# Performance work log

Measured on AMD Instinct MI355X. Metric: run time of the kernel, lower is better.

The kernel has to match this reference:

```python
import jax, jax.numpy as jnp
import numpy as np

HEADS = 12
LN_EPS = 1e-5


def setup_inputs() -> dict:
    B, S, D = 2, 2048, 768
    k = jax.random.key(0)
    ks = jax.random.split(k, 16)
    std = 0.02
    inp = {
        "key": jax.random.normal(ks[0], (B, S, D), jnp.float32),
        "query": jax.random.normal(ks[1], (B, S, D), jnp.float32),
        "value": jax.random.normal(ks[2], (B, S, D), jnp.float32),
        "mask": jax.random.randint(ks[3], (B, S, S), 0, 2).astype(bool),
        "Wk_w": jax.random.normal(ks[4], (D, D), jnp.float32) * std,
        "Wk_b": jnp.zeros((D,), jnp.float32),
        "Wq_w": jax.random.normal(ks[5], (D, D), jnp.float32) * std,
        "Wq_b": jnp.zeros((D,), jnp.float32),
        "Wv_w": jax.random.normal(ks[6], (D, D), jnp.float32) * std,
        "Wv_b": jnp.zeros((D,), jnp.float32),
        "Wc_w": jax.random.normal(ks[7], (D, D), jnp.float32) * std,
        "Wc_b": jnp.zeros((D,), jnp.float32),
        "ln_g": jnp.ones((D,), jnp.float32),
        "ln_b": jnp.zeros((D,), jnp.float32),
    }
    return inp


def _mha(key, query, value, mask, Wk_w, Wk_b, Wq_w, Wq_b, Wv_w, Wv_b,
         Wc_w, Wc_b, ln_g, ln_b):
    B, Sq, D = query.shape
    Sk = key.shape[1]
    H = HEADS
    hd = D // H
    scaler = np.float32(D ** 0.5)  # NOTE: source scales by sqrt(hidden_size), not sqrt(head_dim)

    # QKV projections (torch Linear: x @ W.T + b)
    hk = (key @ Wk_w.T + Wk_b).reshape(B, Sk, H, hd).transpose(2, 0, 1, 3)    # (H,B,Sk,hd)
    hq = (query @ Wq_w.T + Wq_b).reshape(B, Sq, H, hd).transpose(2, 0, 1, 3)  # (H,B,Sq,hd)
    hv = (value @ Wv_w.T + Wv_b).reshape(B, Sk, H, hd).transpose(2, 0, 1, 3)  # (H,B,Sk,hd)

    qk = jnp.einsum('hbqd,hbkd->hbqk', hq, hk) / scaler
    qk = jnp.where(mask[None], -jnp.inf, qk)  # mask repeated over heads in source
    attn = jax.nn.softmax(qk, axis=-1)        # dropout is identity in eval
    out = jnp.einsum('hbqk,hbkd->hbqd', attn, hv)  # (H,B,Sq,hd)

    # Faithful replication of source reshape chain:
    # (H*B,Sq,hd).view(B,H,Sq,hd).permute(1,2,0,3).view(B,Sq,D)
    out = out.reshape(B, H, Sq, hd)             # flat reinterpretation, head-major data
    out = jnp.transpose(out, (1, 2, 0, 3)).reshape(B, Sq, D)

    out = out @ Wc_w.T + Wc_b                   # Wconcat; dropout identity
    x = out + query                             # residual
    mu = jnp.mean(x, axis=-1, keepdims=True)
    var = jnp.mean((x - mu) ** 2, axis=-1, keepdims=True)
    return ln_g * (x - mu) / jnp.sqrt(var + LN_EPS) + ln_b


def reference(key, query, value, mask, Wk_w, Wk_b, Wq_w, Wq_b, Wv_w, Wv_b,
              Wc_w, Wc_b, ln_g, ln_b):
    return _mha(key, query, value, mask, Wk_w, Wk_b, Wq_w, Wq_b,
                Wv_w, Wv_b, Wc_w, Wc_b, ln_g, ln_b)
```

## Files before the change

kernel.cpp:

```cpp
#include <hip/hip_runtime.h>
#include <stdint.h>

typedef float v4f __attribute__((ext_vector_type(4)));
typedef short v8s __attribute__((ext_vector_type(8)));

#define AS1 __attribute__((address_space(1)))
#define AS3 __attribute__((address_space(3)))

__device__ __forceinline__ void load16_to_lds(const void* g, void* l) {
  __builtin_amdgcn_global_load_lds((AS1 void*)g, (AS3 void*)l, 16, 0, 0);
}

__device__ __forceinline__ float fexp2(float x) {
#if __has_builtin(__builtin_amdgcn_exp2f)
  return __builtin_amdgcn_exp2f(x);
#else
  return exp2f(x);
#endif
}

__device__ __forceinline__ unsigned short f2bf_rn(float f) {
  union { float f; uint32_t u; } v; v.f = f;
  return (unsigned short)((v.u + 0x8000u) >> 16);
}
__device__ __forceinline__ uint32_t pack_bf2(float x, float y) {
  union { float f; uint32_t u; } a, b; a.f = x; b.f = y;
  return __builtin_amdgcn_perm(b.u + 0x8000u, a.u + 0x8000u, 0x07060302u);
}

#define QSCALE 0.052058786f

__global__ __launch_bounds__(256) void conv_pack_kernel(
    const float* __restrict__ wk, const float* __restrict__ wq,
    const float* __restrict__ wv, const float* __restrict__ wc,
    const float* __restrict__ kin, const float* __restrict__ qin,
    const float* __restrict__ vin, const uint32_t* __restrict__ mask,
    unsigned short* __restrict__ dk, unsigned short* __restrict__ dq,
    unsigned short* __restrict__ dv, unsigned short* __restrict__ dc,
    unsigned short* __restrict__ dki, unsigned short* __restrict__ dqi,
    unsigned short* __restrict__ dvi, uint32_t* __restrict__ bits) {
  const int id = blockIdx.x;
  const int tid = threadIdx.x;
  if (id >= 11520) {
    const int xx = id - 11520;
    __shared__ int s_i32;
    if (tid == 0) s_i32 = 1;
    __syncthreads();
    if (mask[tid] > 1u) s_i32 = 0;
    __syncthreads();
    if (s_i32) {
      const int lane = tid & 63;
      const int gw = (xx * 256 + tid) >> 6;
#pragma unroll 4
      for (int it = 0; it < 32; ++it) {
        const size_t base = (size_t)gw * 2048 + it * 64;
        unsigned long long bal = __ballot(mask[base + lane] != 0u);
        if (lane == 0) *(unsigned long long*)&bits[base >> 5] = bal;
      }
    } else {
      const int wi = xx * 256 + tid;
      const uint32_t* p = mask + (size_t)wi * 8;
      uint32_t w = 0;
#pragma unroll
      for (int j8 = 0; j8 < 8; ++j8) {
        uint32_t u = p[j8];
#pragma unroll
        for (int k = 0; k < 4; ++k)
          w |= (((u >> (8 * k)) & 0xFFu) ? 1u : 0u) << (j8 * 4 + k);
      }
      bits[wi] = w;
    }
    return;
  }
  const float* s; unsigned short* d; float sc = 1.f; int x;
  if (id < 2304) {
    const int y = id / 576;
    x = id - y * 576;
    if (y == 0)      { s = wk; d = dk; }
    else if (y == 1) { s = wq; d = dq; sc = QSCALE; }
    else if (y == 2) { s = wv; d = dv; }
    else             { s = wc; d = dc; }
  } else {
    const int t = id - 2304;
    const int y = t / 3072;
    x = t - y * 3072;
    if (y == 0)      { s = kin; d = dki; }
    else if (y == 1) { s = qin; d = dqi; }
    else             { s = vin; d = dvi; }
  }
  const int i = x * 256 + tid;
  float4 f = ((const float4*)s)[i];
  uint2 o;
  o.x = pack_bf2(f.x * sc, f.y * sc);
  o.y = pack_bf2(f.z * sc, f.w * sc);
  ((uint2*)d)[i] = o;
}

__global__ __launch_bounds__(256, 3) void gemm_qkv_kernel(
    const unsigned short* __restrict__ qin, const unsigned short* __restrict__ kin,
    const unsigned short* __restrict__ vin,
    const unsigned short* __restrict__ wqb, const unsigned short* __restrict__ wkb,
    const unsigned short* __restrict__ wvb,
    const float* __restrict__ bq, const float* __restrict__ bk,
    const float* __restrict__ bv,
    unsigned short* __restrict__ Qb, unsigned short* __restrict__ Kb,
    unsigned short* __restrict__ Vt) {
  const int which = blockIdx.z;
  const unsigned short* A; const unsigned short* Wb; const float* bias;
  float bscale = 1.f;
  if (which == 0)      { A = qin; Wb = wqb; bias = bq; bscale = QSCALE; }
  else if (which == 1) { A = kin; Wb = wkb; bias = bk; }
  else                 { A = vin; Wb = wvb; bias = bv; }

  const int m0 = blockIdx.x * 128, n0 = blockIdx.y * 128;
  const int tid = threadIdx.x, lane = tid & 63, wid = tid >> 6;
  const int wm = wid >> 1, wn = wid & 1;
  const int l16 = lane & 15, quad = lane >> 4;

  __shared__ __align__(16) unsigned short As[2][128 * 32];
  __shared__ __align__(16) unsigned short Bs[2][128 * 32];

  v4f acc[4][4];
#pragma unroll
  for (int i = 0; i < 4; ++i)
#pragma unroll
    for (int j = 0; j < 4; ++j) { v4f z = {0.f, 0.f, 0.f, 0.f}; acc[i][j] = z; }

  const int c0 = wid * 128 + lane, c1 = wid * 128 + 64 + lane;
  const unsigned short* a0 = A + (size_t)(m0 + (c0 >> 2)) * 768 + (c0 & 3) * 8;
  const unsigned short* a1 = A + (size_t)(m0 + (c1 >> 2)) * 768 + (c1 & 3) * 8;
  const unsigned short* b0 = Wb + (size_t)(n0 + (c0 >> 2)) * 768 + (c0 & 3) * 8;
  const unsigned short* b1 = Wb + (size_t)(n0 + (c1 >> 2)) * 768 + (c1 & 3) * 8;

#define QKV_STAGE(k0, buf)                                         \
  do {                                                             \
    load16_to_lds(a0 + (k0), &As[buf][(wid * 128) * 8]);           \
    load16_to_lds(a1 + (k0), &As[buf][(wid * 128 + 64) * 8]);      \
    load16_to_lds(b0 + (k0), &Bs[buf][(wid * 128) * 8]);           \
    load16_to_lds(b1 + (k0), &Bs[buf][(wid * 128 + 64) * 8]);      \
  } while (0)

  QKV_STAGE(0, 0);
#pragma unroll 2
  for (int ks = 0; ks < 24; ++ks) {
    const int bufc = ks & 1;
    __syncthreads();
    v8s af[4], bf[4];
#pragma unroll
    for (int i = 0; i < 4; ++i)
      af[i] = *(const v8s*)&As[bufc][(wm * 64 + i * 16 + l16) * 32 + quad * 8];
#pragma unroll
    for (int j = 0; j < 4; ++j)
      bf[j] = *(const v8s*)&Bs[bufc][(wn * 64 + j * 16 + l16) * 32 + quad * 8];
    if (ks < 23) QKV_STAGE((ks + 1) * 32, bufc ^ 1);
#pragma unroll
    for (int i = 0; i < 4; ++i)
#pragma unroll
      for (int j = 0; j < 4; ++j)
        acc[i][j] = __builtin_amdgcn_mfma_f32_16x16x32_bf16(af[i], bf[j],
                                                            acc[i][j], 0, 0, 0);
  }
#undef QKV_STAGE

#pragma unroll
  for (int i = 0; i < 4; ++i) {
#pragma unroll
    for (int j = 0; j < 4; ++j) {
      const int mbase = m0 + wm * 64 + i * 16 + quad * 4;
      const int n = n0 + wn * 64 + j * 16 + l16;
      const float bv_ = bias[n] * bscale;
      if (which == 2) {
        const int bb = mbase >> 11, ss = mbase & 2047;
        uint2 pk;
        pk.x = pack_bf2(acc[i][j][0] + bv_, acc[i][j][1] + bv_);
        pk.y = pack_bf2(acc[i][j][2] + bv_, acc[i][j][3] + bv_);
        *(uint2*)&Vt[((size_t)bb * 768 + n) * 2048 + ss] = pk;
      } else {
        unsigned short* dst = (which == 0) ? Qb : Kb;
#pragma unroll
        for (int r = 0; r < 4; ++r)
          dst[(size_t)(mbase + r) * 768 + n] = f2bf_rn(acc[i][j][r] + bv_);
      }
    }
  }
}

__global__ __launch_bounds__(256, 4) void attn_kernel(
    const unsigned short* __restrict__ Qb, const unsigned short* __restrict__ Kb,
    const unsigned short* __restrict__ Vt, const uint32_t* __restrict__ mbits,
    unsigned short* __restrict__ X) {
  const int q0 = blockIdx.x * 64;
  const int h = blockIdx.y, b = blockIdx.z;
  const int tid = threadIdx.x, w = tid >> 6, lane = tid & 63;
  const int l16 = lane & 15, quad = lane >> 4, l7 = l16 & 7;

  __shared__ __align__(16) unsigned short Kl[2][64 * 64];
  __shared__ __align__(16) unsigned short Vl[2][64 * 64];
  __shared__ __align__(16) unsigned short Pl[4][16 * 64];

  v8s aq[2];
  {
    const unsigned short* qp =
        Qb + (size_t)(b * 2048 + q0 + w * 16 + l16) * 768 + h * 64 + quad * 8;
    aq[0] = *(const v8s*)qp;
    aq[1] = *(const v8s*)(qp + 32);
  }

  v4f o[4], ol;
#pragma unroll
  for (int nt = 0; nt < 4; ++nt) { v4f z = {0.f, 0.f, 0.f, 0.f}; o[nt] = z; }
  { v4f z = {0.f, 0.f, 0.f, 0.f}; ol = z; }

  v8s bones;
  {
    const short v1 = (l16 == 0) ? (short)0x3F80 : (short)0;
#pragma unroll
    for (int j = 0; j < 8; ++j) bones[j] = v1;
  }

  const int rsub = lane >> 3;
  const int csub = ((lane & 7) ^ rsub) * 8;
  const unsigned short* kg0 = Kb + (size_t)(b * 2048 + w * 16) * 768 + h * 64;
  const unsigned short* vg0 = Vt + (size_t)(b * 768 + h * 64 + w * 16) * 2048;
  const uint2* mp =
      (const uint2*)(mbits + (size_t)(b * 2048 + q0 + w * 16 + l16) * 64);

#define ATTN_STAGE(kk0, buf)                                                   \
  do {                                                                         \
    const unsigned short* kg = kg0 + (size_t)(kk0) * 768;                      \
    const unsigned short* vg = vg0 + (kk0);                                    \
    load16_to_lds(kg + (size_t)rsub * 768 + csub, &Kl[buf][(w * 16) * 64]);    \
    load16_to_lds(kg + (size_t)(8 + rsub) * 768 + csub,                        \
                  &Kl[buf][(w * 16 + 8) * 64]);                                \
    load16_to_lds(vg + (size_t)rsub * 2048 + csub, &Vl[buf][(w * 16) * 64]);   \
    load16_to_lds(vg + (size_t)(8 + rsub) * 2048 + csub,                       \
                  &Vl[buf][(w * 16 + 8) * 64]);                                \
  } while (0)

  ATTN_STAGE(0, 0);
  uint2 mreg = mp[0];
#pragma unroll 2
  for (int it = 0; it < 32; ++it) {
    const int bufc = it & 1;
    __syncthreads();

    v8s bk[2][4];
#pragma unroll
    for (int kt = 0; kt < 2; ++kt)
#pragma unroll
      for (int nt = 0; nt < 4; ++nt)
        bk[kt][nt] = *(const v8s*)&Kl[bufc][(nt * 16 + l16) * 64 +
                                           (((kt * 4 + quad) ^ l7) << 3)];
    uint2 mnext;
    if (it < 31) {
      ATTN_STAGE((it + 1) * 64, bufc ^ 1);
      mnext = mp[it + 1];
    }

    v4f sacc[4];
#pragma unroll
    for (int nt = 0; nt < 4; ++nt) { v4f z = {0.f, 0.f, 0.f, 0.f}; sacc[nt] = z; }
#pragma unroll
    for (int kt = 0; kt < 2; ++kt)
#pragma unroll
      for (int nt = 0; nt < 4; ++nt)
        sacc[nt] = __builtin_amdgcn_mfma_f32_16x16x32_bf16(bk[kt][nt], aq[kt],
                                                           sacc[nt], 0, 0, 0);

    const uint32_t u[4] = {mreg.x >> (quad * 4), mreg.x >> (quad * 4 + 16),
                           mreg.y >> (quad * 4), mreg.y >> (quad * 4 + 16)};
#pragma unroll
    for (int nt = 0; nt < 4; ++nt) {
      const float p0 = (u[nt] & 1u) ? 0.f : fexp2(sacc[nt][0]);
      const float p1 = ((u[nt] >> 1) & 1u) ? 0.f : fexp2(sacc[nt][1]);
      const float p2 = ((u[nt] >> 2) & 1u) ? 0.f : fexp2(sacc[nt][2]);
      const float p3 = ((u[nt] >> 3) & 1u) ? 0.f : fexp2(sacc[nt][3]);
      uint2 pk;
      pk.x = pack_bf2(p0, p1);
      pk.y = pack_bf2(p2, p3);
      const int elem =
          l16 * 64 + (((nt * 2 + (quad >> 1)) ^ l7) << 3) + (quad & 1) * 4;
      *(uint2*)&Pl[w][elem] = pk;
    }

#pragma unroll
    for (int kt = 0; kt < 2; ++kt) {
      const v8s ap = *(const v8s*)&Pl[w][l16 * 64 + (((kt * 4 + quad) ^ l7) << 3)];
#pragma unroll
      for (int nt = 0; nt < 4; ++nt) {
        const v8s bv = *(const v8s*)&Vl[bufc][(nt * 16 + l16) * 64 +
                                             (((kt * 4 + quad) ^ l7) << 3)];
        o[nt] = __builtin_amdgcn_mfma_f32_16x16x32_bf16(ap, bv, o[nt], 0, 0, 0);
      }
      ol = __builtin_amdgcn_mfma_f32_16x16x32_bf16(ap, bones, ol, 0, 0, 0);
    }
    mreg = mnext;
  }
#undef ATTN_STAGE

  const int hb2 = 2 * h + b;
  const int b2 = (hb2 >= 12) ? 1 : 0;
  const int h2 = hb2 - 12 * b2;
#pragma unroll
  for (int r = 0; r < 4; ++r) {
    const float lsum = __shfl(ol[r], quad * 16, 64);
    const float inv_l = 1.f / lsum;
    const int q = q0 + w * 16 + quad * 4 + r;
#pragma unroll
    for (int nt = 0; nt < 4; ++nt) {
      const int d = nt * 16 + l16;
      const size_t f = (size_t)h2 * 262144 + (size_t)q * 128 + b2 * 64 + d;
      X[f] = f2bf_rn(o[nt][r] * inv_l);
    }
  }
}

__global__ __launch_bounds__(256, 3) void gemm2_kernel(
    const unsigned short* __restrict__ X, const unsigned short* __restrict__ Wcb,
    const float* __restrict__ bc, const float* __restrict__ query,
    float* __restrict__ out) {
  const int m0 = blockIdx.x * 64, n0 = blockIdx.y * 128;
  const int tid = threadIdx.x, lane = tid & 63, wid = tid >> 6;
  const int wm = wid >> 1, wn = wid & 1;
  const int l16 = lane & 15, quad = lane >> 4;

  __shared__ __align__(16) unsigned short As[2][64 * 32];
  __shared__ __align__(16) unsigned short Bs[2][128 * 32];

  v4f acc[2][4];
#pragma unroll
  for (int i = 0; i < 2; ++i)
#pragma unroll
    for (int j = 0; j < 4; ++j) { v4f z = {0.f, 0.f, 0.f, 0.f}; acc[i][j] = z; }

  const int ca = tid;
  const unsigned short* a0 = X + (size_t)(m0 + (ca >> 2)) * 768 + (ca & 3) * 8;
  const int c0 = wid * 128 + lane, c1 = wid * 128 + 64 + lane;
  const unsigned short* b0 = Wcb + (size_t)(n0 + (c0 >> 2)) * 768 + (c0 & 3) * 8;
  const unsigned short* b1 = Wcb + (size_t)(n0 + (c1 >> 2)) * 768 + (c1 & 3) * 8;

#define G2_STAGE(k0, buf)                                        \
  do {                                                           \
    load16_to_lds(a0 + (k0), &As[buf][(wid * 64) * 8]);          \
    load16_to_lds(b0 + (k0), &Bs[buf][(wid * 128) * 8]);         \
    load16_to_lds(b1 + (k0), &Bs[buf][(wid * 128 + 64) * 8]);    \
  } while (0)

  G2_STAGE(0, 0);
#pragma unroll 2
  for (int ks = 0; ks < 24; ++ks) {
    const int bufc = ks & 1;
    __syncthreads();
    v8s af[2], bf[4];
#pragma unroll
    for (int i = 0; i < 2; ++i)
      af[i] = *(const v8s*)&As[bufc][(wm * 32 + i * 16 + l16) * 32 + quad * 8];
#pragma unroll
    for (int j = 0; j < 4; ++j)
      bf[j] = *(const v8s*)&Bs[bufc][(wn * 64 + j * 16 + l16) * 32 + quad * 8];
    if (ks < 23) G2_STAGE((ks + 1) * 32, bufc ^ 1);
#pragma unroll
    for (int i = 0; i < 2; ++i)
#pragma unroll
      for (int j = 0; j < 4; ++j)
        acc[i][j] = __builtin_amdgcn_mfma_f32_16x16x32_bf16(af[i], bf[j],
                                                            acc[i][j], 0, 0, 0);
  }
#undef G2_STAGE

#pragma unroll
  for (int i = 0; i < 2; ++i) {
#pragma unroll
    for (int j = 0; j < 4; ++j) {
      const int mbase = m0 + wm * 32 + i * 16 + quad * 4;
      const int n = n0 + wn * 64 + j * 16 + l16;
      const float bv_ = bc[n];
#pragma unroll
      for (int r = 0; r < 4; ++r) {
        const int m = mbase + r;
        out[(size_t)m * 768 + n] =
            acc[i][j][r] + bv_ + query[(size_t)m * 768 + n];
      }
    }
  }
}

__global__ __launch_bounds__(256) void ln_kernel(float* __restrict__ out,
                                                 const float* __restrict__ g,
                                                 const float* __restrict__ bta) {
  const int row = blockIdx.x;
  const int tid = threadIdx.x;
  float x[3];
  float s = 0.f, sq = 0.f;
#pragma unroll
  for (int k = 0; k < 3; ++k) {
    x[k] = out[(size_t)row * 768 + tid + k * 256];
    s += x[k];
    sq += x[k] * x[k];
  }
#pragma unroll
  for (int off = 1; off < 64; off <<= 1) {
    s += __shfl_xor(s, off, 64);
    sq += __shfl_xor(sq, off, 64);
  }
  __shared__ float ss[4], ssq[4];
  const int w = tid >> 6, lane = tid & 63;
  if (lane == 0) { ss[w] = s; ssq[w] = sq; }
  __syncthreads();
  s = ss[0] + ss[1] + ss[2] + ss[3];
  sq = ssq[0] + ssq[1] + ssq[2] + ssq[3];
  const float mu = s * (1.f / 768.f);
  const float var = sq * (1.f / 768.f) - mu * mu;
  const float rstd = rsqrtf(var + 1e-5f);
#pragma unroll
  for (int k = 0; k < 3; ++k) {
    const int cc = tid + k * 256;
    out[(size_t)row * 768 + cc] = g[cc] * (x[k] - mu) * rstd + bta[cc];
  }
}

extern "C" void kernel_launch(void* const* d_in, const int* in_sizes, int n_in,
                              void* d_out, int out_size, void* d_ws,
                              size_t ws_size, hipStream_t stream) {
  const float* key   = (const float*)d_in[0];
  const float* query = (const float*)d_in[1];
  const float* value = (const float*)d_in[2];
  const uint32_t* mask = (const uint32_t*)d_in[3];
  const float* Wk = (const float*)d_in[4];
  const float* bk = (const float*)d_in[5];
  const float* Wq = (const float*)d_in[6];
  const float* bq = (const float*)d_in[7];
  const float* Wv = (const float*)d_in[8];
  const float* bv = (const float*)d_in[9];
  const float* Wc = (const float*)d_in[10];
  const float* bc = (const float*)d_in[11];
  const float* lng = (const float*)d_in[12];
  const float* lnb = (const float*)d_in[13];

  char* ws = (char*)d_ws;
  uint32_t*       mbits = (uint32_t*)(ws);
  unsigned short* Wkb = (unsigned short*)(ws + 0x100000);
  unsigned short* Wqb = (unsigned short*)(ws + 0x220000);
  unsigned short* Wvb = (unsigned short*)(ws + 0x340000);
  unsigned short* Wcb = (unsigned short*)(ws + 0x460000);
  unsigned short* Qb  = (unsigned short*)(ws + 0x600000);
  unsigned short* Kb  = (unsigned short*)(ws + 0xC00000);
  unsigned short* Vt  = (unsigned short*)(ws + 0x1200000);
  unsigned short* X   = (unsigned short*)(ws + 0x1800000);
  unsigned short* Kin = (unsigned short*)d_out;
  unsigned short* Qin = (unsigned short*)d_out + 3145728;
  unsigned short* Vin = X;
  float* out = (float*)d_out;

  conv_pack_kernel<<<dim3(12544), dim3(256), 0, stream>>>(
      Wk, Wq, Wv, Wc, key, query, value, mask,
      Wkb, Wqb, Wvb, Wcb, Kin, Qin, Vin, mbits);
  gemm_qkv_kernel<<<dim3(32, 6, 3), dim3(256), 0, stream>>>(
      Qin, Kin, Vin, Wqb, Wkb, Wvb, bq, bk, bv, Qb, Kb, Vt);
  attn_kernel<<<dim3(32, 12, 2), dim3(256), 0, stream>>>(Qb, Kb, Vt, mbits, X);
  gemm2_kernel<<<dim3(64, 6), dim3(256), 0, stream>>>(X, Wcb, bc, query, out);
  ln_kernel<<<dim3(4096), dim3(256), 0, stream>>>(out, lng, lnb);
}
```

Baseline: 241.2 us.

## Fuse fp32-to-bf16 conversion and mask packing into QKV and output GEMMs

Removes the separate conversion kernel. The QKV and output-projection GEMMs now read fp32 activations and weights straight from global memory into registers, convert them to bf16 and store them into LDS, with a register-prefetched double buffer. Mask bit-packing moves into an extra z-slice of the QKV grid. For V the operand roles are swapped so the transposed Vt is written along contiguous rows. This saves one launch and a full bf16 round trip through memory. In exchange the GEMM mainloops do more register and VALU work, lose the async global-to-LDS loads, and Vt is now written as scalar 16-bit stores.

```diff
diff --git a/kernel.cpp b/kernel.cpp
--- a/kernel.cpp
+++ b/kernel.cpp
@@ -30,90 +30,57 @@
 
 #define QSCALE 0.052058786f
 
-__global__ __launch_bounds__(256) void conv_pack_kernel(
-    const float* __restrict__ wk, const float* __restrict__ wq,
-    const float* __restrict__ wv, const float* __restrict__ wc,
-    const float* __restrict__ kin, const float* __restrict__ qin,
-    const float* __restrict__ vin, const uint32_t* __restrict__ mask,
-    unsigned short* __restrict__ dk, unsigned short* __restrict__ dq,
-    unsigned short* __restrict__ dv, unsigned short* __restrict__ dc,
-    unsigned short* __restrict__ dki, unsigned short* __restrict__ dqi,
-    unsigned short* __restrict__ dvi, uint32_t* __restrict__ bits) {
-  const int id = blockIdx.x;
+__global__ __launch_bounds__(256, 3) void gemm_qkv_kernel(
+    const float* __restrict__ qin, const float* __restrict__ kin,
+    const float* __restrict__ vin,
+    const float* __restrict__ Wq, const float* __restrict__ Wk,
+    const float* __restrict__ Wv,
+    const float* __restrict__ bq, const float* __restrict__ bk,
+    const float* __restrict__ bv, const uint32_t* __restrict__ mask,
+    unsigned short* __restrict__ Qb, unsigned short* __restrict__ Kb,
+    unsigned short* __restrict__ Vt, uint32_t* __restrict__ bits) {
   const int tid = threadIdx.x;
-  if (id >= 11520) {
-    const int xx = id - 11520;
+  if (blockIdx.z == 3) {
     __shared__ int s_i32;
     if (tid == 0) s_i32 = 1;
     __syncthreads();
     if (mask[tid] > 1u) s_i32 = 0;
     __syncthreads();
-    if (s_i32) {
-      const int lane = tid & 63;
-      const int gw = (xx * 256 + tid) >> 6;
+    const int lane = tid & 63;
+    for (int g = blockIdx.x + 32 * blockIdx.y; g < 1024; g += 192) {
+      if (s_i32) {
+        const int gw = (g * 256 + tid) >> 6;
 #pragma unroll 4
-      for (int it = 0; it < 32; ++it) {
-        const size_t base = (size_t)gw * 2048 + it * 64;
-        unsigned long long bal = __ballot(mask[base + lane] != 0u);
-        if (lane == 0) *(unsigned long long*)&bits[base >> 5] = bal;
+        for (int it2 = 0; it2 < 32; ++it2) {
+          const size_t base = (size_t)gw * 2048 + it2 * 64;
+          unsigned long long bal = __ballot(mask[base + lane] != 0u);
+          if (lane == 0) *(unsigned long long*)&bits[base >> 5] = bal;
+        }
+      } else {
+        const int wi = g * 256 + tid;
+        const uint32_t* p = mask + (size_t)wi * 8;
+        uint32_t w = 0;
+#pragma unroll
+        for (int j8 = 0; j8 < 8; ++j8) {
+          uint32_t u = p[j8];
+#pragma unroll
+          for (int k = 0; k < 4; ++k)
+            w |= (((u >> (8 * k)) & 0xFFu) ? 1u : 0u) << (j8 * 4 + k);
+        }
+        bits[wi] = w;
       }
-    } else {
-      const int wi = xx * 256 + tid;
-      const uint32_t* p = mask + (size_t)wi * 8;
-      uint32_t w = 0;
-#pragma unroll
-      for (int j8 = 0; j8 < 8; ++j8) {
-        uint32_t u = p[j8];
-#pragma unroll
-        for (int k = 0; k < 4; ++k)
-          w |= (((u >> (8 * k)) & 0xFFu) ? 1u : 0u) << (j8 * 4 + k);
-      }
-      bits[wi] = w;
     }
     return;
   }
-  const float* s; unsigned short* d; float sc = 1.f; int x;
-  if (id < 2304) {
-    const int y = id / 576;
-    x = id - y * 576;
-    if (y == 0)      { s = wk; d = dk; }
-    else if (y == 1) { s = wq; d = dq; sc = QSCALE; }
-    else if (y == 2) { s = wv; d = dv; }
-    else             { s = wc; d = dc; }
-  } else {
-    const int t = id - 2304;
-    const int y = t / 3072;
-    x = t - y * 3072;
-    if (y == 0)      { s = kin; d = dki; }
-    else if (y == 1) { s = qin; d = dqi; }
-    else             { s = vin; d = dvi; }
-  }
-  const int i = x * 256 + tid;
-  float4 f = ((const float4*)s)[i];
-  uint2 o;
-  o.x = pack_bf2(f.x * sc, f.y * sc);
-  o.y = pack_bf2(f.z * sc, f.w * sc);
-  ((uint2*)d)[i] = o;
-}
-
-__global__ __launch_bounds__(256, 3) void gemm_qkv_kernel(
-    const unsigned short* __restrict__ qin, const unsigned short* __restrict__ kin,
-    const unsigned short* __restrict__ vin,
-    const unsigned short* __restrict__ wqb, const unsigned short* __restrict__ wkb,
-    const unsigned short* __restrict__ wvb,
-    const float* __restrict__ bq, const float* __restrict__ bk,
-    const float* __restrict__ bv,
-    unsigned short* __restrict__ Qb, unsigned short* __restrict__ Kb,
-    unsigned short* __restrict__ Vt) {
+
   const int which = blockIdx.z;
-  const unsigned short* A; const unsigned short* Wb; const float* bias;
-  float bscale = 1.f;
-  if (which == 0)      { A = qin; Wb = wqb; bias = bq; bscale = QSCALE; }
-  else if (which == 1) { A = kin; Wb = wkb; bias = bk; }
-  else                 { A = vin; Wb = wvb; bias = bv; }
+  const float* A; const float* W; const float* bias; float wsc = 1.f;
+  if (which == 0)      { A = qin; W = Wq; bias = bq; wsc = QSCALE; }
+  else if (which == 1) { A = kin; W = Wk; bias = bk; }
+  else                 { A = vin; W = Wv; bias = bv; }
 
   const int m0 = blockIdx.x * 128, n0 = blockIdx.y * 128;
-  const int tid = threadIdx.x, lane = tid & 63, wid = tid >> 6;
+  const int lane = tid & 63, wid = tid >> 6;
   const int wm = wid >> 1, wn = wid & 1;
   const int l16 = lane & 15, quad = lane >> 4;
 
@@ -126,57 +93,98 @@
 #pragma unroll
     for (int j = 0; j < 4; ++j) { v4f z = {0.f, 0.f, 0.f, 0.f}; acc[i][j] = z; }
 
-  const int c0 = wid * 128 + lane, c1 = wid * 128 + 64 + lane;
-  const unsigned short* a0 = A + (size_t)(m0 + (c0 >> 2)) * 768 + (c0 & 3) * 8;
-  const unsigned short* a1 = A + (size_t)(m0 + (c1 >> 2)) * 768 + (c1 & 3) * 8;
-  const unsigned short* b0 = Wb + (size_t)(n0 + (c0 >> 2)) * 768 + (c0 & 3) * 8;
-  const unsigned short* b1 = Wb + (size_t)(n0 + (c1 >> 2)) * 768 + (c1 & 3) * 8;
-
-#define QKV_STAGE(k0, buf)                                         \
-  do {                                                             \
-    load16_to_lds(a0 + (k0), &As[buf][(wid * 128) * 8]);           \
-    load16_to_lds(a1 + (k0), &As[buf][(wid * 128 + 64) * 8]);      \
-    load16_to_lds(b0 + (k0), &Bs[buf][(wid * 128) * 8]);           \
-    load16_to_lds(b1 + (k0), &Bs[buf][(wid * 128 + 64) * 8]);      \
+  const float* pA[2]; const float* pW[2]; int offs[2];
+#pragma unroll
+  for (int i = 0; i < 2; ++i) {
+    const int c = tid + i * 256;
+    const int row = c >> 2, col8 = (c & 3) * 8;
+    pA[i] = A + (size_t)(m0 + row) * 768 + col8;
+    pW[i] = W + (size_t)(n0 + row) * 768 + col8;
+    offs[i] = row * 32 + col8;
+  }
+
+  float4 fa[2][2], fw[2][2];
+#define QKV_LOAD(k0)                                      \
+  do {                                                    \
+    _Pragma("unroll") for (int i = 0; i < 2; ++i) {       \
+      fa[i][0] = *(const float4*)(pA[i] + (k0));          \
+      fa[i][1] = *(const float4*)(pA[i] + (k0) + 4);      \
+      fw[i][0] = *(const float4*)(pW[i] + (k0));          \
+      fw[i][1] = *(const float4*)(pW[i] + (k0) + 4);      \
+    }                                                     \
   } while (0)
-
-  QKV_STAGE(0, 0);
+#define QKV_STORE(buf)                                                   \
+  do {                                                                   \
+    _Pragma("unroll") for (int i = 0; i < 2; ++i) {                      \
+      uint4 oa, ow;                                                      \
+      oa.x = pack_bf2(fa[i][0].x, fa[i][0].y);                           \
+      oa.y = pack_bf2(fa[i][0].z, fa[i][0].w);                           \
+      oa.z = pack_bf2(fa[i][1].x, fa[i][1].y);                           \
+      oa.w = pack_bf2(fa[i][1].z, fa[i][1].w);                           \
+      ow.x = pack_bf2(fw[i][0].x * wsc, fw[i][0].y * wsc);               \
+      ow.y = pack_bf2(fw[i][0].z * wsc, fw[i][0].w * wsc);               \
+      ow.z = pack_bf2(fw[i][1].x * wsc, fw[i][1].y * wsc);               \
+      ow.w = pack_bf2(fw[i][1].z * wsc, fw[i][1].w * wsc);               \
+      *(uint4*)&As[buf][offs[i]] = oa;                                   \
+      *(uint4*)&Bs[buf][offs[i]] = ow;                                   \
+    }                                                                    \
+  } while (0)
+
+  QKV_LOAD(0);
+  QKV_STORE(0);
+  QKV_LOAD(32);
 #pragma unroll 2
   for (int ks = 0; ks < 24; ++ks) {
     const int bufc = ks & 1;
     __syncthreads();
     v8s af[4], bf[4];
+    const unsigned short* Abase = (which == 2) ? Bs[bufc] : As[bufc];
+    const unsigned short* Bbase = (which == 2) ? As[bufc] : Bs[bufc];
 #pragma unroll
     for (int i = 0; i < 4; ++i)
-      af[i] = *(const v8s*)&As[bufc][(wm * 64 + i * 16 + l16) * 32 + quad * 8];
+      af[i] = *(const v8s*)&Abase[(wm * 64 + i * 16 + l16) * 32 + quad * 8];
 #pragma unroll
     for (int j = 0; j < 4; ++j)
-      bf[j] = *(const v8s*)&Bs[bufc][(wn * 64 + j * 16 + l16) * 32 + quad * 8];
-    if (ks < 23) QKV_STAGE((ks + 1) * 32, bufc ^ 1);
+      bf[j] = *(const v8s*)&Bbase[(wn * 64 + j * 16 + l16) * 32 + quad * 8];
+    if (ks < 23) QKV_STORE(bufc ^ 1);
 #pragma unroll
     for (int i = 0; i < 4; ++i)
 #pragma unroll
       for (int j = 0; j < 4; ++j)
         acc[i][j] = __builtin_amdgcn_mfma_f32_16x16x32_bf16(af[i], bf[j],
                                                             acc[i][j], 0, 0, 0);
-  }
-#undef QKV_STAGE
-
-#pragma unroll
-  for (int i = 0; i < 4; ++i) {
-#pragma unroll
-    for (int j = 0; j < 4; ++j) {
-      const int mbase = m0 + wm * 64 + i * 16 + quad * 4;
-      const int n = n0 + wn * 64 + j * 16 + l16;
-      const float bv_ = bias[n] * bscale;
-      if (which == 2) {
-        const int bb = mbase >> 11, ss = mbase & 2047;
-        uint2 pk;
-        pk.x = pack_bf2(acc[i][j][0] + bv_, acc[i][j][1] + bv_);
-        pk.y = pack_bf2(acc[i][j][2] + bv_, acc[i][j][3] + bv_);
-        *(uint2*)&Vt[((size_t)bb * 768 + n) * 2048 + ss] = pk;
-      } else {
-        unsigned short* dst = (which == 0) ? Qb : Kb;
+    if (ks < 22) QKV_LOAD((ks + 2) * 32);
+  }
+#undef QKV_LOAD
+#undef QKV_STORE
+
+  if (which == 2) {
+    const int bb = m0 >> 11;
+#pragma unroll
+    for (int i = 0; i < 4; ++i) {
+#pragma unroll
+      for (int j = 0; j < 4; ++j) {
+        const int nbase = n0 + wm * 64 + i * 16 + quad * 4;
+        const int mcol = m0 + wn * 64 + j * 16 + l16;
+        const int ss = mcol & 2047;
+#pragma unroll
+        for (int r = 0; r < 4; ++r) {
+          const int n = nbase + r;
+          Vt[((size_t)bb * 768 + n) * 2048 + ss] =
+              f2bf_rn(acc[i][j][r] + bias[n]);
+        }
+      }
+    }
+  } else {
+    unsigned short* dst = (which == 0) ? Qb : Kb;
+    const float bscale = (which == 0) ? QSCALE : 1.f;
+#pragma unroll
+    for (int i = 0; i < 4; ++i) {
+#pragma unroll
+      for (int j = 0; j < 4; ++j) {
+        const int mbase = m0 + wm * 64 + i * 16 + quad * 4;
+        const int n = n0 + wn * 64 + j * 16 + l16;
+        const float bv_ = bias[n] * bscale;
 #pragma unroll
         for (int r = 0; r < 4; ++r)
           dst[(size_t)(mbase + r) * 768 + n] = f2bf_rn(acc[i][j][r] + bv_);
@@ -316,7 +324,7 @@
 }
 
 __global__ __launch_bounds__(256, 3) void gemm2_kernel(
-    const unsigned short* __restrict__ X, const unsigned short* __restrict__ Wcb,
+    const unsigned short* __restrict__ X, const float* __restrict__ Wc,
     const float* __restrict__ bc, const float* __restrict__ query,
     float* __restrict__ out) {
   const int m0 = blockIdx.x * 64, n0 = blockIdx.y * 128;
@@ -333,20 +341,40 @@
 #pragma unroll
     for (int j = 0; j < 4; ++j) { v4f z = {0.f, 0.f, 0.f, 0.f}; acc[i][j] = z; }
 
-  const int ca = tid;
-  const unsigned short* a0 = X + (size_t)(m0 + (ca >> 2)) * 768 + (ca & 3) * 8;
-  const int c0 = wid * 128 + lane, c1 = wid * 128 + 64 + lane;
-  const unsigned short* b0 = Wcb + (size_t)(n0 + (c0 >> 2)) * 768 + (c0 & 3) * 8;
-  const unsigned short* b1 = Wcb + (size_t)(n0 + (c1 >> 2)) * 768 + (c1 & 3) * 8;
-
-#define G2_STAGE(k0, buf)                                        \
-  do {                                                           \
-    load16_to_lds(a0 + (k0), &As[buf][(wid * 64) * 8]);          \
-    load16_to_lds(b0 + (k0), &Bs[buf][(wid * 128) * 8]);         \
-    load16_to_lds(b1 + (k0), &Bs[buf][(wid * 128 + 64) * 8]);    \
+  const unsigned short* a0 = X + (size_t)(m0 + (tid >> 2)) * 768 + (tid & 3) * 8;
+  const float* pW[2]; int offs[2];
+#pragma unroll
+  for (int i = 0; i < 2; ++i) {
+    const int c = tid + i * 256;
+    const int row = c >> 2, col8 = (c & 3) * 8;
+    pW[i] = Wc + (size_t)(n0 + row) * 768 + col8;
+    offs[i] = row * 32 + col8;
+  }
+
+  float4 fw[2][2];
+#define G2_LOAD(k0)                                       \
+  do {                                                    \
+    _Pragma("unroll") for (int i = 0; i < 2; ++i) {       \
+      fw[i][0] = *(const float4*)(pW[i] + (k0));          \
+      fw[i][1] = *(const float4*)(pW[i] + (k0) + 4);      \
+    }                                                     \
   } while (0)
-
-  G2_STAGE(0, 0);
+#define G2_STORE(buf)                                                    \
+  do {                                                                   \
+    _Pragma("unroll") for (int i = 0; i < 2; ++i) {                      \
+      uint4 ow;                                                          \
+      ow.x = pack_bf2(fw[i][0].x, fw[i][0].y);                           \
+      ow.y = pack_bf2(fw[i][0].z, fw[i][0].w);                           \
+      ow.z = pack_bf2(fw[i][1].x, fw[i][1].y);                           \
+      ow.w = pack_bf2(fw[i][1].z, fw[i][1].w);                           \
+      *(uint4*)&Bs[buf][offs[i]] = ow;                                   \
+    }                                                                    \
+  } while (0)
+
+  G2_LOAD(0);
+  G2_STORE(0);
+  load16_to_lds(a0, &As[0][(wid * 64) * 8]);
+  G2_LOAD(32);
 #pragma unroll 2
   for (int ks = 0; ks < 24; ++ks) {
     const int bufc = ks & 1;
@@ -358,15 +386,20 @@
 #pragma unroll
     for (int j = 0; j < 4; ++j)
       bf[j] = *(const v8s*)&Bs[bufc][(wn * 64 + j * 16 + l16) * 32 + quad * 8];
-    if (ks < 23) G2_STAGE((ks + 1) * 32, bufc ^ 1);
+    if (ks < 23) {
+      G2_STORE(bufc ^ 1);
+      load16_to_lds(a0 + (ks + 1) * 32, &As[bufc ^ 1][(wid * 64) * 8]);
+    }
 #pragma unroll
     for (int i = 0; i < 2; ++i)
 #pragma unroll
       for (int j = 0; j < 4; ++j)
         acc[i][j] = __builtin_amdgcn_mfma_f32_16x16x32_bf16(af[i], bf[j],
                                                             acc[i][j], 0, 0, 0);
-  }
-#undef G2_STAGE
+    if (ks < 22) G2_LOAD((ks + 2) * 32);
+  }
+#undef G2_LOAD
+#undef G2_STORE
 
 #pragma unroll
   for (int i = 0; i < 2; ++i) {
@@ -439,25 +472,15 @@
 
   char* ws = (char*)d_ws;
   uint32_t*       mbits = (uint32_t*)(ws);
-  unsigned short* Wkb = (unsigned short*)(ws + 0x100000);
-  unsigned short* Wqb = (unsigned short*)(ws + 0x220000);
-  unsigned short* Wvb = (unsigned short*)(ws + 0x340000);
-  unsigned short* Wcb = (unsigned short*)(ws + 0x460000);
-  unsigned short* Qb  = (unsigned short*)(ws + 0x600000);
-  unsigned short* Kb  = (unsigned short*)(ws + 0xC00000);
-  unsigned short* Vt  = (unsigned short*)(ws + 0x1200000);
-  unsigned short* X   = (unsigned short*)(ws + 0x1800000);
-  unsigned short* Kin = (unsigned short*)d_out;
-  unsigned short* Qin = (unsigned short*)d_out + 3145728;
-  unsigned short* Vin = X;
+  unsigned short* Qb = (unsigned short*)(ws + 0x100000);
+  unsigned short* Kb = (unsigned short*)(ws + 0x700000);
+  unsigned short* Vt = (unsigned short*)(ws + 0xD00000);
+  unsigned short* X  = (unsigned short*)(ws + 0x1300000);
   float* out = (float*)d_out;
 
-  conv_pack_kernel<<<dim3(12544), dim3(256), 0, stream>>>(
-      Wk, Wq, Wv, Wc, key, query, value, mask,
-      Wkb, Wqb, Wvb, Wcb, Kin, Qin, Vin, mbits);
-  gemm_qkv_kernel<<<dim3(32, 6, 3), dim3(256), 0, stream>>>(
-      Qin, Kin, Vin, Wqb, Wkb, Wvb, bq, bk, bv, Qb, Kb, Vt);
+  gemm_qkv_kernel<<<dim3(32, 6, 4), dim3(256), 0, stream>>>(
+      query, key, value, Wq, Wk, Wv, bq, bk, bv, mask, Qb, Kb, Vt, mbits);
   attn_kernel<<<dim3(32, 12, 2), dim3(256), 0, stream>>>(Qb, Kb, Vt, mbits, X);
-  gemm2_kernel<<<dim3(64, 6), dim3(256), 0, stream>>>(X, Wcb, bc, query, out);
+  gemm2_kernel<<<dim3(64, 6), dim3(256), 0, stream>>>(X, Wc, bc, query, out);
   ln_kernel<<<dim3(4096), dim3(256), 0, stream>>>(out, lng, lnb);
 }
```

After: 296.4 us. +22.9%, slower.
